# Optimization experiments

Measured on AMD Instinct MI355X. Metric: run time of the kernel, lower is better.

The kernel has to match this reference:

```python
import jax, jax.numpy as jnp
import numpy as np

T, R, L = 3, 4, 2            # node types, edge relations, HGT layers
H, D = 8, 16                 # heads, head dim
OUT = H * D                  # 128
IN = 128
N_T = 30000                  # nodes per type
E = 200000                   # edges per relation
EDGE_SRC = (0, 0, 1, 0)      # src node type of each relation
EDGE_DST = (0, 1, 0, 2)      # dst node type of each relation


def segment_softmax(logits, seg, num_seg):
    # softmax over edges grouped by destination node (per head)
    m = jax.ops.segment_max(logits, seg, num_segments=num_seg)
    m = jnp.where(jnp.isfinite(m), m, 0.0)
    e = jnp.exp(logits - m[seg])
    ssum = jax.ops.segment_sum(e, seg, num_segments=num_seg)
    return e / (ssum[seg] + 1e-16)


def hgt_layer(hs, edge_index, k_w, k_b, q_w, q_b, v_w, v_b, a_w, a_b, skip, a_rel, m_rel, p_rel):
    # per-node-type K/Q/V projections, [N_t, H, D]
    k = [(hs[t] @ k_w[t] + k_b[t]).reshape(-1, H, D) for t in range(T)]
    q = [(hs[t] @ q_w[t] + q_b[t]).reshape(-1, H, D) for t in range(T)]
    v = [(hs[t] @ v_w[t] + v_b[t]).reshape(-1, H, D) for t in range(T)]
    agg = [jnp.zeros((hs[t].shape[0], OUT), hs[t].dtype) for t in range(T)]
    inv_sqrt_d = 1.0 / np.sqrt(D).astype(np.float32)
    for r in range(R):
        s, d = EDGE_SRC[r], EDGE_DST[r]
        src, dst = edge_index[r, 0], edge_index[r, 1]
        # relation-specific transforms of source K and V
        k_rel = jnp.einsum('nhd,hde->nhe', k[s], a_rel[r])
        v_rel = jnp.einsum('nhd,hde->nhe', v[s], m_rel[r])
        k_j = k_rel[src]           # [E, H, D]
        v_j = v_rel[src]           # [E, H, D]
        q_i = q[d][dst]            # [E, H, D]
        logits = (q_i * k_j).sum(-1) * p_rel[r] * inv_sqrt_d   # [E, H]
        n_d = hs[d].shape[0]
        alpha = segment_softmax(logits, dst, n_d)              # [E, H]
        msg = (v_j * alpha[..., None]).reshape(-1, OUT)        # [E, OUT]
        agg[d] = agg[d] + jax.ops.segment_sum(msg, dst, num_segments=n_d)
    out = []
    for t in range(T):
        o = jax.nn.gelu(agg[t], approximate=False) @ a_w[t] + a_b[t]
        a_s = jax.nn.sigmoid(skip[t])
        out.append(a_s * o + (1.0 - a_s) * hs[t])   # learnable skip (dims match)
    return out


def _forward(x_t0, x_t1, x_t2, x_homo, lin_w, lin_b, k_w, k_b, q_w, q_b, v_w, v_b,
             a_w, a_b, skip, a_rel, m_rel, p_rel, edge_index, node_type_argmax):
    xs = [x_t0, x_t1, x_t2]
    # type-specific input projection + ReLU
    hs = [jax.nn.relu(xs[t] @ lin_w[t] + lin_b[t]) for t in range(T)]
    for l in range(L):
        hs = hgt_layer(hs, edge_index, k_w[l], k_b[l], q_w[l], q_b[l], v_w[l], v_b[l],
                       a_w[l], a_b[l], skip[l], a_rel[l], m_rel[l], p_rel[l])
    # hetero_to_homo_features: scatter per-type rows back to global node order
    num_nodes = x_homo.shape[0]
    h = jnp.zeros((num_nodes, OUT), hs[0].dtype)
    for t in range(T):
        mask = node_type_argmax == t
        local = jnp.clip(jnp.cumsum(mask) - 1, 0, hs[t].shape[0] - 1)
        h = jnp.where(mask[:, None], hs[t][local], h)
    return h


def setup_inputs() -> dict:
    key = jax.random.key(0)
    ks = jax.random.split(key, 16)
    w = 0.05
    return {
        'x_t0': jax.random.normal(ks[0], (N_T, IN), jnp.float32),
        'x_t1': jax.random.normal(ks[1], (N_T, IN), jnp.float32),
        'x_t2': jax.random.normal(ks[2], (N_T, IN), jnp.float32),
        'x_homo': jax.random.normal(ks[3], (T * N_T, IN), jnp.float32),
        'lin_w': jax.random.normal(ks[4], (T, IN, OUT), jnp.float32) * w,
        'lin_b': jnp.zeros((T, OUT), jnp.float32),
        'k_w': jax.random.normal(ks[5], (L, T, OUT, OUT), jnp.float32) * w,
        'k_b': jnp.zeros((L, T, OUT), jnp.float32),
        'q_w': jax.random.normal(ks[6], (L, T, OUT, OUT), jnp.float32) * w,
        'q_b': jnp.zeros((L, T, OUT), jnp.float32),
        'v_w': jax.random.normal(ks[7], (L, T, OUT, OUT), jnp.float32) * w,
        'v_b': jnp.zeros((L, T, OUT), jnp.float32),
        'a_w': jax.random.normal(ks[8], (L, T, OUT, OUT), jnp.float32) * w,
        'a_b': jnp.zeros((L, T, OUT), jnp.float32),
        'skip': jnp.ones((L, T), jnp.float32),
        'a_rel': jax.random.normal(ks[9], (L, R, H, D, D), jnp.float32) * 0.2,
        'm_rel': jax.random.normal(ks[10], (L, R, H, D, D), jnp.float32) * 0.2,
        'p_rel': jnp.ones((L, R, H), jnp.float32),
        'edge_index': jax.random.randint(ks[11], (R, 2, E), 0, N_T),
        'node_type_argmax': jnp.repeat(jnp.arange(T), N_T),
    }


def reference(x_t0, x_t1, x_t2, x_homo, lin_w, lin_b, k_w, k_b, q_w, q_b, v_w, v_b,
              a_w, a_b, skip, a_rel, m_rel, p_rel, edge_index, node_type_argmax):
    return _forward(x_t0, x_t1, x_t2, x_homo, lin_w, lin_b, k_w, k_b, q_w, q_b,
                    v_w, v_b, a_w, a_b, skip, a_rel, m_rel, p_rel,
                    edge_index, node_type_argmax)
```

## Files before the change

### kernel.cpp

```cpp
#include <hip/hip_runtime.h>
#include <math.h>

#define NT_NODES 30000
#define NE_EDGES 200000
#define NTY 3
#define NRL 4
#define NLY 2
#define NH 8
#define HD 16
#define FDIM 128
#define SCAN_BLOCKS 118

typedef unsigned short u16;
typedef unsigned int u32;
typedef __attribute__((ext_vector_type(8))) short bf16x8;
typedef __attribute__((ext_vector_type(4))) float f32x4;

__device__ __forceinline__ float bf2f(u16 u) {
  return __uint_as_float(((u32)u) << 16);
}
__device__ __forceinline__ u16 f2bf(float f) {
  u32 u = __float_as_uint(f);
  return (u16)((u + 0x7FFFu + ((u >> 16) & 1u)) >> 16);
}

__device__ __forceinline__ float gelu_f(float x) {
  return 0.5f * x * (1.f + erff(x * 0.7071067811865475f));
}

struct WtBatch { const float* w[23]; };
__global__ __launch_bounds__(256) void wt_prep(WtBatch wb, u16* wt) {
  const float* w = wb.w[blockIdx.x];
  u16* o = wt + (size_t)blockIdx.x * FDIM * FDIM;
  for (int i = threadIdx.x; i < FDIM * FDIM; i += 256) {
    int n = i >> 7, k = i & 127;
    o[i] = f2bf(w[(size_t)k * FDIM + n]);
  }
}


struct QkvOut { const u16* WT; const float* bias; u16* C; int ldc; };
struct QkvTask { const u16* A; int nout; QkvOut o[3]; };
struct QkvBatch { QkvTask t[3]; };

__global__ __launch_bounds__(256) void gemm_qkv(QkvBatch gb, int M) {
  const QkvTask tk = gb.t[blockIdx.z];
  const int tid = threadIdx.x;
  const int wv = tid >> 6;
  const int lane = tid & 63;
  const int row0 = blockIdx.x * 64;

  __shared__ u16 As[64 * 128];
  __shared__ u16 Bt[128 * 128];

  #pragma unroll
  for (int i = 0; i < 4; i++) {
    int g = tid + 256 * i;
    int r = g >> 4, k8 = g & 15;
    int grow = row0 + r;
    uint4 v = make_uint4(0, 0, 0, 0);
    if (grow < M) v = *(const uint4*)(tk.A + (size_t)grow * FDIM + k8 * 8);
    *(uint4*)(As + r * 128 + ((k8 ^ (r & 7)) * 8)) = v;
  }
  __syncthreads();

  const int rsel = lane & 15, ksel = lane >> 4;
  bf16x8 af[4][4];
  #pragma unroll
  for (int ks = 0; ks < 4; ks++) {
    int kg = ks * 4 + ksel;
    #pragma unroll
    for (int i = 0; i < 4; i++) {
      int r = 16 * i + rsel;
      af[ks][i] = *(const bf16x8*)(As + r * 128 + ((kg ^ (r & 7)) * 8));
    }
  }

  for (int ot = 0; ot < tk.nout; ot++) {
    const QkvOut oo = tk.o[ot];
    #pragma unroll
    for (int i = 0; i < 8; i++) {
      int g = tid + 256 * i;
      int n = g >> 4, k8 = g & 15;
      uint4 v = *(const uint4*)(oo.WT + (size_t)n * FDIM + k8 * 8);
      *(uint4*)(Bt + n * 128 + ((k8 ^ (n & 7)) * 8)) = v;
    }
    __syncthreads();

    f32x4 acc[4][2] = {};
    #pragma unroll
    for (int ks = 0; ks < 4; ks++) {
      int kg = ks * 4 + ksel;
      bf16x8 bfr[2];
      #pragma unroll
      for (int j = 0; j < 2; j++) {
        int n = 32 * wv + 16 * j + rsel;
        bfr[j] = *(const bf16x8*)(Bt + n * 128 + ((kg ^ (n & 7)) * 8));
      }
      #pragma unroll
      for (int i = 0; i < 4; i++)
        #pragma unroll
        for (int j = 0; j < 2; j++)
          acc[i][j] = __builtin_amdgcn_mfma_f32_16x16x32_bf16(af[ks][i], bfr[j], acc[i][j], 0, 0, 0);
    }

    const int ldc = oo.ldc;
    float bj[2];
    int colj[2];
    #pragma unroll
    for (int j = 0; j < 2; j++) {
      colj[j] = 32 * wv + 16 * j + rsel;
      bj[j] = oo.bias[colj[j]];
    }
    #pragma unroll
    for (int i = 0; i < 4; i++) {
      #pragma unroll
      for (int rr = 0; rr < 4; rr++) {
        int grow = row0 + 16 * i + (lane >> 4) * 4 + rr;
        if (grow >= M) continue;
        #pragma unroll
        for (int j = 0; j < 2; j++)
          oo.C[(size_t)grow * ldc + colj[j]] = f2bf(acc[i][j][rr] + bj[j]);
      }
    }
    __syncthreads();
  }
}

struct GemmTaskF {
  const float* A; const float* A2; const u16* WT; const float* bias;
  float* C; const u16* oldh; const float* skipp;
};
struct GemmBatchF { GemmTaskF t[3]; };

template<int GELU_A, int EPI_SKIP, int RELU, int BF16_OUT>
__global__ __launch_bounds__(256) void gemm_mfma_f(GemmBatchF gb, int M) {
  const GemmTaskF tk = gb.t[blockIdx.z];
  const int tid = threadIdx.x;
  const int wv = tid >> 6;
  const int lane = tid & 63;
  const int row0 = blockIdx.x * 64;

  __shared__ u16 As[64 * 128];
  __shared__ u16 Bt[128 * 128];

  #pragma unroll
  for (int i = 0; i < 4; i++) {
    int g = tid + 256 * i;
    int r = g >> 4, k8 = g & 15;
    int grow = row0 + r;
    float4 va = make_float4(0.f, 0.f, 0.f, 0.f), vb = va;
    if (grow < M) {
      const float* ap = tk.A + (size_t)grow * FDIM + k8 * 8;
      va = *(const float4*)ap;
      vb = *(const float4*)(ap + 4);
      if (GELU_A && tk.A2) {
        const float* ap2 = tk.A2 + (size_t)grow * FDIM + k8 * 8;
        float4 w = *(const float4*)ap2;
        float4 z = *(const float4*)(ap2 + 4);
        va.x += w.x; va.y += w.y; va.z += w.z; va.w += w.w;
        vb.x += z.x; vb.y += z.y; vb.z += z.z; vb.w += z.w;
      }
      if (GELU_A) {
        va.x = gelu_f(va.x); va.y = gelu_f(va.y); va.z = gelu_f(va.z); va.w = gelu_f(va.w);
        vb.x = gelu_f(vb.x); vb.y = gelu_f(vb.y); vb.z = gelu_f(vb.z); vb.w = gelu_f(vb.w);
      }
    }
    u32 w0 = (u32)f2bf(va.x) | ((u32)f2bf(va.y) << 16);
    u32 w1 = (u32)f2bf(va.z) | ((u32)f2bf(va.w) << 16);
    u32 w2 = (u32)f2bf(vb.x) | ((u32)f2bf(vb.y) << 16);
    u32 w3 = (u32)f2bf(vb.z) | ((u32)f2bf(vb.w) << 16);
    u32* dst = (u32*)(As + r * 128 + ((k8 ^ (r & 7)) * 8));
    dst[0] = w0; dst[1] = w1; dst[2] = w2; dst[3] = w3;
  }
  #pragma unroll
  for (int i = 0; i < 8; i++) {
    int g = tid + 256 * i;
    int n = g >> 4, k8 = g & 15;
    uint4 v = *(const uint4*)(tk.WT + (size_t)n * FDIM + k8 * 8);
    *(uint4*)(Bt + n * 128 + ((k8 ^ (n & 7)) * 8)) = v;
  }
  __syncthreads();

  f32x4 acc[4][2] = {};
  const int rsel = lane & 15, ksel = lane >> 4;
  #pragma unroll
  for (int ks = 0; ks < 4; ks++) {
    int kg = ks * 4 + ksel;
    bf16x8 af[4], bfr[2];
    #pragma unroll
    for (int i = 0; i < 4; i++) {
      int r = 16 * i + rsel;
      af[i] = *(const bf16x8*)(As + r * 128 + ((kg ^ (r & 7)) * 8));
    }
    #pragma unroll
    for (int j = 0; j < 2; j++) {
      int n = 32 * wv + 16 * j + rsel;
      bfr[j] = *(const bf16x8*)(Bt + n * 128 + ((kg ^ (n & 7)) * 8));
    }
    #pragma unroll
    for (int i = 0; i < 4; i++)
      #pragma unroll
      for (int j = 0; j < 2; j++)
        acc[i][j] = __builtin_amdgcn_mfma_f32_16x16x32_bf16(af[i], bfr[j], acc[i][j], 0, 0, 0);
  }

  float a_s = 0.f, b_s = 0.f;
  if (EPI_SKIP) { a_s = 1.f / (1.f + expf(-tk.skipp[0])); b_s = 1.f - a_s; }
  float bj[2];
  int colj[2];
  #pragma unroll
  for (int j = 0; j < 2; j++) {
    colj[j] = 32 * wv + 16 * j + rsel;
    bj[j] = tk.bias[colj[j]];
  }
  #pragma unroll
  for (int i = 0; i < 4; i++) {
    #pragma unroll
    for (int rr = 0; rr < 4; rr++) {
      int grow = row0 + 16 * i + (lane >> 4) * 4 + rr;
      if (grow >= M) continue;
      #pragma unroll
      for (int j = 0; j < 2; j++) {
        float v = acc[i][j][rr] + bj[j];
        if (RELU) v = fmaxf(v, 0.f);
        if (EPI_SKIP) v = a_s * v + b_s * bf2f(tk.oldh[(size_t)grow * FDIM + colj[j]]);
        if (BF16_OUT) ((u16*)tk.C)[(size_t)grow * FDIM + colj[j]] = f2bf(v);
        else tk.C[(size_t)grow * FDIM + colj[j]] = v;
      }
    }
  }
}

__global__ __launch_bounds__(256) void csr_hist(const int* __restrict__ edge_index,
                                                int* __restrict__ counts) {
  int idx = blockIdx.x * 256 + threadIdx.x;
  if (idx >= NRL * NE_EDGES) return;
  int r = idx / NE_EDGES, e = idx - r * NE_EDGES;
  int d = edge_index[(size_t)(r * 2 + 1) * NE_EDGES + e];
  atomicAdd(&counts[r * NT_NODES + d], 1);
}

__global__ __launch_bounds__(256) void scan_block(const int* __restrict__ counts,
                                                  int* __restrict__ off,
                                                  int* __restrict__ aux) {
  int r = blockIdx.y, b = blockIdx.x, t = threadIdx.x;
  int i = b * 256 + t;
  int v = (i < NT_NODES) ? counts[r * NT_NODES + i] : 0;
  __shared__ int lds[256];
  lds[t] = v;
  __syncthreads();
  #pragma unroll
  for (int dlt = 1; dlt < 256; dlt <<= 1) {
    int x = (t >= dlt) ? lds[t - dlt] : 0;
    __syncthreads();
    lds[t] += x;
    __syncthreads();
  }
  if (i < NT_NODES) off[(size_t)r * (NT_NODES + 1) + i] = lds[t] - v;
  if (t == 255) aux[r * SCAN_BLOCKS + b] = lds[255];
}

__global__ __launch_bounds__(128) void scan_aux(const int* __restrict__ aux,
                                                int* __restrict__ auxe,
                                                int* __restrict__ off) {
  int r = blockIdx.x, t = threadIdx.x;
  __shared__ int lds[128];
  int v = (t < SCAN_BLOCKS) ? aux[r * SCAN_BLOCKS + t] : 0;
  lds[t] = v;
  __syncthreads();
  #pragma unroll
  for (int dlt = 1; dlt < 128; dlt <<= 1) {
    int x = (t >= dlt) ? lds[t - dlt] : 0;
    __syncthreads();
    lds[t] += x;
    __syncthreads();
  }
  if (t < SCAN_BLOCKS) auxe[r * SCAN_BLOCKS + t] = lds[t] - v;
  if (t == 127) off[(size_t)r * (NT_NODES + 1) + NT_NODES] = lds[127];
}

__global__ __launch_bounds__(256) void scan_add(const int* __restrict__ auxe,
                                                int* __restrict__ off,
                                                int* __restrict__ cursor) {
  int r = blockIdx.y, b = blockIdx.x, t = threadIdx.x;
  int i = b * 256 + t;
  if (i >= NT_NODES) return;
  int val = off[(size_t)r * (NT_NODES + 1) + i] + auxe[r * SCAN_BLOCKS + b];
  off[(size_t)r * (NT_NODES + 1) + i] = val;
  cursor[r * NT_NODES + i] = val;
}

__global__ __launch_bounds__(256) void csr_scatter(const int* __restrict__ edge_index,
                                                   int* __restrict__ cursor,
                                                   int* __restrict__ csr_src) {
  int idx = blockIdx.x * 256 + threadIdx.x;
  if (idx >= NRL * NE_EDGES) return;
  int r = idx / NE_EDGES, e = idx - r * NE_EDGES;
  int s = edge_index[(size_t)(r * 2 + 0) * NE_EDGES + e];
  int d = edge_index[(size_t)(r * 2 + 1) * NE_EDGES + e];
  int pos = atomicAdd(&cursor[r * NT_NODES + d], 1);
  csr_src[(size_t)r * NE_EDGES + pos] = s;
}

__global__ void csr_pad(int* __restrict__ pad) {
  if (threadIdx.x < 8) pad[threadIdx.x] = 0;
}

struct AttnRel {
  const int* csr_src; const int* off;
  const u16* q;
  const u16* kv;
  const float* Arel;
  const float* Mrel;
  const float* prel;
  float* agg;
};
struct AttnBatch { AttnRel r[4]; };

__global__ __launch_bounds__(256) void attn_fused(AttnBatch ab) {
  const AttnRel rp = ab.r[blockIdx.y];
  const int wave = threadIdx.x >> 6;
  const int lane = threadIdx.x & 63;
  const int d = blockIdx.x * 2 + (wave >> 1);
  if (d >= NT_NODES) return;
  const int hf = wave & 1;
  const int cl = lane & 15;
  const int gh = hf * 4 + (lane >> 4);
  const int grp = lane & ~15;
  const int el = lane & 7;

  float qv = bf2f(rp.q[(size_t)d * FDIM + hf * 64 + lane]);
  const float* A = rp.Arel + (size_t)gh * 256;
  float qp = 0.f;
  #pragma unroll
  for (int ee = 0; ee < 16; ee++) {
    float qe = __shfl(qv, grp + ee, 64);
    qp += A[cl * 16 + ee] * qe;
  }
  qp *= rp.prel[gh] * 0.25f;

  const u16* KV = rp.kv;
  const int* __restrict__ cs = rp.csr_src;
  int lo = rp.off[d], hi = rp.off[d + 1];
  lo = __builtin_amdgcn_readfirstlane(lo);
  hi = __builtin_amdgcn_readfirstlane(hi);
  const size_t koff = hf * 64 + lane;
  const size_t voff = 128 + hf * 64 + lane;
  float acc = 0.f, ssum = 0.f;
  for (int pos = lo; pos < hi; pos += 8) {
    int s0 = cs[pos + 0], s1 = cs[pos + 1], s2 = cs[pos + 2], s3 = cs[pos + 3];
    int s4 = cs[pos + 4], s5 = cs[pos + 5], s6 = cs[pos + 6], s7 = cs[pos + 7];
    u16 k0 = KV[(size_t)s0 * 256 + koff], k1 = KV[(size_t)s1 * 256 + koff];
    u16 k2 = KV[(size_t)s2 * 256 + koff], k3 = KV[(size_t)s3 * 256 + koff];
    u16 k4 = KV[(size_t)s4 * 256 + koff], k5 = KV[(size_t)s5 * 256 + koff];
    u16 k6 = KV[(size_t)s6 * 256 + koff], k7 = KV[(size_t)s7 * 256 + koff];
    u16 v0 = KV[(size_t)s0 * 256 + voff], v1 = KV[(size_t)s1 * 256 + voff];
    u16 v2 = KV[(size_t)s2 * 256 + voff], v3 = KV[(size_t)s3 * 256 + voff];
    u16 v4 = KV[(size_t)s4 * 256 + voff], v5 = KV[(size_t)s5 * 256 + voff];
    u16 v6 = KV[(size_t)s6 * 256 + voff], v7 = KV[(size_t)s7 * 256 + voff];
    float p0 = qp * bf2f(k0), p1 = qp * bf2f(k1);
    float p2 = qp * bf2f(k2), p3 = qp * bf2f(k3);
    float p4 = qp * bf2f(k4), p5 = qp * bf2f(k5);
    float p6 = qp * bf2f(k6), p7 = qp * bf2f(k7);
    float s01 = (lane & 1) ? p0 : p1, c01 = (lane & 1) ? p1 : p0;
    float s23 = (lane & 1) ? p2 : p3, c23 = (lane & 1) ? p3 : p2;
    float s45 = (lane & 1) ? p4 : p5, c45 = (lane & 1) ? p5 : p4;
    float s67 = (lane & 1) ? p6 : p7, c67 = (lane & 1) ? p7 : p6;
    float r01 = c01 + __shfl_xor(s01, 1, 64);
    float r23 = c23 + __shfl_xor(s23, 1, 64);
    float r45 = c45 + __shfl_xor(s45, 1, 64);
    float r67 = c67 + __shfl_xor(s67, 1, 64);
    float sA = (lane & 2) ? r01 : r23, cA = (lane & 2) ? r23 : r01;
    float sB = (lane & 2) ? r45 : r67, cB = (lane & 2) ? r67 : r45;
    float rA = cA + __shfl_xor(sA, 2, 64);
    float rB = cB + __shfl_xor(sB, 2, 64);
    float sC = (lane & 4) ? rA : rB, cC = (lane & 4) ? rB : rA;
    float rF = cC + __shfl_xor(sC, 4, 64);
    rF += __shfl_xor(rF, 8, 64);
    int rem = hi - pos;
    float e = (el < rem) ? __expf(rF) : 0.f;
    float e0 = __shfl(e, grp + 0, 64), e1 = __shfl(e, grp + 1, 64);
    float e2 = __shfl(e, grp + 2, 64), e3 = __shfl(e, grp + 3, 64);
    float e4 = __shfl(e, grp + 4, 64), e5 = __shfl(e, grp + 5, 64);
    float e6 = __shfl(e, grp + 6, 64), e7 = __shfl(e, grp + 7, 64);
    acc += e0 * bf2f(v0) + e1 * bf2f(v1) + e2 * bf2f(v2) + e3 * bf2f(v3)
         + e4 * bf2f(v4) + e5 * bf2f(v5) + e6 * bf2f(v6) + e7 * bf2f(v7);
    ssum += ((e0 + e1) + (e2 + e3)) + ((e4 + e5) + (e6 + e7));
  }
  float inv = 1.f / (ssum + 1e-16f);
  float S = acc * inv;

  const float* M = rp.Mrel + (size_t)gh * 256;
  float o = 0.f;
  #pragma unroll
  for (int d2 = 0; d2 < 16; d2++) {
    float sv = __shfl(S, grp + d2, 64);
    o += sv * M[d2 * 16 + cl];
  }
  rp.agg[(size_t)d * FDIM + hf * 64 + lane] = o;
}

__global__ __launch_bounds__(256) void scatter_out(const float* h0, const float* h1,
                                                   const float* h2, const int* ntype,
                                                   float* out, int NN) {
  int idx = blockIdx.x * 256 + threadIdx.x;
  if (idx >= NN * 32) return;
  int i = idx >> 5, c4 = idx & 31;
  int t = ntype[i];
  const float* hp = (t == 0) ? h0 : ((t == 1) ? h1 : h2);
  int local = i - t * NT_NODES;
  ((float4*)out)[idx] = ((const float4*)hp)[(size_t)local * 32 + c4];
}

static const int ESRC[NRL] = {0, 0, 1, 0};
static const int EDST[NRL] = {0, 1, 0, 2};

extern "C" void kernel_launch(void* const* d_in, const int* in_sizes, int n_in,
                              void* d_out, int out_size, void* d_ws, size_t ws_size,
                              hipStream_t stream) {
  const float* x[3] = {(const float*)d_in[0], (const float*)d_in[1], (const float*)d_in[2]};
  const float* lin_w = (const float*)d_in[4];
  const float* lin_b = (const float*)d_in[5];
  const float* k_w   = (const float*)d_in[6];
  const float* k_b   = (const float*)d_in[7];
  const float* q_w   = (const float*)d_in[8];
  const float* q_b   = (const float*)d_in[9];
  const float* v_w   = (const float*)d_in[10];
  const float* v_b   = (const float*)d_in[11];
  const float* a_w   = (const float*)d_in[12];
  const float* a_b   = (const float*)d_in[13];
  const float* skip  = (const float*)d_in[14];
  const float* a_rel = (const float*)d_in[15];
  const float* m_rel = (const float*)d_in[16];
  const float* p_rel = (const float*)d_in[17];
  const int* edge_index = (const int*)d_in[18];
  const int* ntype   = (const int*)d_in[19];
  float* out = (float*)d_out;

  const size_t NF = (size_t)NT_NODES * FDIM;
  float* p = (float*)d_ws;
  auto alloc = [&](size_t n) { float* r = p; p += n; return r; };
  float* bufA = alloc(3 * NF);
  float* bufB = alloc(3 * NF);
  float* agg  = alloc(3 * NF);
  float* aggX = alloc(NF);
  u16* kv0 = (u16*)alloc(NF);
  u16* kv1 = (u16*)alloc(NF);
  u16* wt  = (u16*)alloc(23 * FDIM * FDIM / 2);
  int* counts  = (int*)(p);
  int* cursor  = counts + NRL * NT_NODES;
  int* offsets = cursor + NRL * NT_NODES;
  int* aux     = offsets + NRL * (NT_NODES + 1);
  int* auxe    = aux + NRL * SCAN_BLOCKS;
  int* csr_src = auxe + NRL * SCAN_BLOCKS;

  const int gemm_gx = (NT_NODES + 63) / 64;

  {
    WtBatch wb{};
    for (int l = 0; l < NLY; l++) {
      for (int t = 0; t < 3; t++)
        wb.w[l * 7 + t] = q_w + (size_t)(l * NTY + t) * FDIM * FDIM;
      wb.w[l * 7 + 3] = k_w + (size_t)(l * NTY + 0) * FDIM * FDIM;
      wb.w[l * 7 + 4] = v_w + (size_t)(l * NTY + 0) * FDIM * FDIM;
      wb.w[l * 7 + 5] = k_w + (size_t)(l * NTY + 1) * FDIM * FDIM;
      wb.w[l * 7 + 6] = v_w + (size_t)(l * NTY + 1) * FDIM * FDIM;
    }
    for (int t = 0; t < 3; t++)
      wb.w[14 + t] = lin_w + (size_t)t * FDIM * FDIM;
    for (int l = 0; l < NLY; l++)
      for (int t = 0; t < 3; t++)
        wb.w[17 + l * 3 + t] = a_w + (size_t)(l * NTY + t) * FDIM * FDIM;
    wt_prep<<<dim3(23), 256, 0, stream>>>(wb, wt);
  }

  hipMemsetAsync(counts, 0, NRL * NT_NODES * sizeof(int), stream);
  csr_hist<<<dim3((NRL * NE_EDGES + 255) / 256), 256, 0, stream>>>(edge_index, counts);
  scan_block<<<dim3(SCAN_BLOCKS, NRL), 256, 0, stream>>>(counts, offsets, aux);
  scan_aux<<<dim3(NRL), 128, 0, stream>>>(aux, auxe, offsets);
  scan_add<<<dim3(SCAN_BLOCKS, NRL), 256, 0, stream>>>(auxe, offsets, cursor);
  csr_scatter<<<dim3((NRL * NE_EDGES + 255) / 256), 256, 0, stream>>>(edge_index, cursor, csr_src);
  csr_pad<<<dim3(1), 64, 0, stream>>>(csr_src + (size_t)NRL * NE_EDGES);

  {
    GemmBatchF gb{};
    for (int t = 0; t < 3; t++) {
      gb.t[t].A = x[t];
      gb.t[t].A2 = nullptr;
      gb.t[t].WT = wt + (size_t)(14 + t) * FDIM * FDIM;
      gb.t[t].bias = lin_b + (size_t)t * FDIM;
      gb.t[t].C = (float*)((u16*)bufA + (size_t)t * NF);
      gb.t[t].oldh = nullptr; gb.t[t].skipp = nullptr;
    }
    gemm_mfma_f<0, 0, 1, 1><<<dim3(gemm_gx, 1, 3), 256, 0, stream>>>(gb, NT_NODES);
  }

  float* cur = bufA;
  float* alt = bufB;
  for (int l = 0; l < NLY; l++) {
    u16* qbf = (u16*)alt;
    const u16* hb = (const u16*)cur;

    {
      QkvBatch gb{};
      gb.t[0].A = hb;  gb.t[0].nout = 3;
      gb.t[0].o[0] = { wt + (size_t)(l * 7 + 0) * FDIM * FDIM, q_b + (size_t)(l * NTY + 0) * FDIM, qbf,            FDIM };
      gb.t[0].o[1] = { wt + (size_t)(l * 7 + 3) * FDIM * FDIM, k_b + (size_t)(l * NTY + 0) * FDIM, kv0,            256 };
      gb.t[0].o[2] = { wt + (size_t)(l * 7 + 4) * FDIM * FDIM, v_b + (size_t)(l * NTY + 0) * FDIM, kv0 + 128,      256 };
      gb.t[1].A = hb + NF;  gb.t[1].nout = 3;
      gb.t[1].o[0] = { wt + (size_t)(l * 7 + 1) * FDIM * FDIM, q_b + (size_t)(l * NTY + 1) * FDIM, qbf + NF,       FDIM };
      gb.t[1].o[1] = { wt + (size_t)(l * 7 + 5) * FDIM * FDIM, k_b + (size_t)(l * NTY + 1) * FDIM, kv1,            256 };
      gb.t[1].o[2] = { wt + (size_t)(l * 7 + 6) * FDIM * FDIM, v_b + (size_t)(l * NTY + 1) * FDIM, kv1 + 128,      256 };
      gb.t[2].A = hb + 2 * NF;  gb.t[2].nout = 1;
      gb.t[2].o[0] = { wt + (size_t)(l * 7 + 2) * FDIM * FDIM, q_b + (size_t)(l * NTY + 2) * FDIM, qbf + 2 * NF,   FDIM };
      gemm_qkv<<<dim3(gemm_gx, 1, 3), 256, 0, stream>>>(gb, NT_NODES);
    }

    {
      AttnBatch ab{};
      for (int r = 0; r < NRL; r++) {
        int dt = EDST[r];
        ab.r[r].csr_src = csr_src + (size_t)r * NE_EDGES;
        ab.r[r].off  = offsets + (size_t)r * (NT_NODES + 1);
        ab.r[r].q    = qbf + (size_t)dt * NF;
        ab.r[r].kv   = (ESRC[r] == 0) ? kv0 : kv1;
        ab.r[r].Arel = a_rel + (size_t)(l * NRL + r) * NH * HD * HD;
        ab.r[r].Mrel = m_rel + (size_t)(l * NRL + r) * NH * HD * HD;
        ab.r[r].prel = p_rel + (size_t)(l * NRL + r) * NH;
        ab.r[r].agg  = (r == 2) ? aggX : (agg + (size_t)dt * NF);
      }
      attn_fused<<<dim3((NT_NODES + 1) / 2, NRL), 256, 0, stream>>>(ab);
    }

    {
      GemmBatchF gb{};
      for (int t = 0; t < 3; t++) {
        gb.t[t].A = agg + (size_t)t * NF;
        gb.t[t].A2 = (t == 0) ? aggX : nullptr;
        gb.t[t].WT = wt + (size_t)(17 + l * 3 + t) * FDIM * FDIM;
        gb.t[t].bias = a_b + (size_t)(l * NTY + t) * FDIM;
        gb.t[t].oldh = hb + (size_t)t * NF;
        gb.t[t].skipp = skip + (size_t)(l * NTY + t);
        if (l == 0) gb.t[t].C = (float*)((u16*)alt + (size_t)t * NF);
        else        gb.t[t].C = alt + (size_t)t * NF;
      }
      if (l == 0) gemm_mfma_f<1, 1, 0, 1><<<dim3(gemm_gx, 1, 3), 256, 0, stream>>>(gb, NT_NODES);
      else        gemm_mfma_f<1, 1, 0, 0><<<dim3(gemm_gx, 1, 3), 256, 0, stream>>>(gb, NT_NODES);
    }
    float* tmp = cur; cur = alt; alt = tmp;
  }

  const int NN = 3 * NT_NODES;
  scatter_out<<<dim3((NN * 32 + 255) / 256), 256, 0, stream>>>(
      cur, cur + NF, cur + 2 * NF, ntype, out, NN);
}
```

Measured before the change: 575.8 us.

## Fold relation attention matrix and prior scale into per-relation Q weights

A new prep kernel multiplies each destination-type Q weight and bias by the relation-specific a_rel matrix and scales it by p_rel/sqrt(D). This produces one fused Q projection per relation. The QKV GEMM now emits four Q outputs, with type 0 producing two of them, and the attention kernel reads the pre-transformed query directly. That drops its per-node shuffle-based 16x16 matvec and its reads of a_rel and p_rel. In exchange it adds one extra 128-wide GEMM output per layer and a larger Q buffer, and the folded weights are rounded to bf16 after the product, which slightly changes numerics.

```diff
diff --git a/kernel.cpp b/kernel.cpp
--- a/kernel.cpp
+++ b/kernel.cpp
@@ -38,9 +38,50 @@
   }
 }
 
+__global__ __launch_bounds__(256) void qfuse(const float* __restrict__ q_w,
+                                             const float* __restrict__ q_b,
+                                             const float* __restrict__ a_rel,
+                                             const float* __restrict__ p_rel,
+                                             u16* __restrict__ wqp,
+                                             float* __restrict__ bqp) {
+  const int lr = blockIdx.x;
+  const int l = lr >> 2, r = lr & 3;
+  const int dt = (r == 1) ? 1 : ((r == 3) ? 2 : 0);
+  const float* qw = q_w + (size_t)(l * NTY + dt) * FDIM * FDIM;
+  const float* qb = q_b + (size_t)(l * NTY + dt) * FDIM;
+  const float* A  = a_rel + (size_t)(l * NRL + r) * NH * HD * HD;
+  const float* pr = p_rel + (size_t)(l * NRL + r) * NH;
+  u16* wo = wqp + (size_t)lr * FDIM * FDIM;
+  float* bo = bqp + (size_t)lr * FDIM;
+
+  __shared__ float As[NH * HD * HD];
+  __shared__ float sh[NH];
+  for (int i = threadIdx.x; i < NH * HD * HD; i += 256) As[i] = A[i];
+  if (threadIdx.x < NH) sh[threadIdx.x] = pr[threadIdx.x] * 0.25f;
+  __syncthreads();
+
+  for (int i = threadIdx.x; i < FDIM * FDIM; i += 256) {
+    int n = i >> 7, k = i & 127;
+    int h = n >> 4, cl = n & 15;
+    float s = 0.f;
+    #pragma unroll
+    for (int ee = 0; ee < HD; ee++)
+      s += qw[(size_t)k * FDIM + h * HD + ee] * As[h * HD * HD + cl * HD + ee];
+    wo[(size_t)n * FDIM + k] = f2bf(s * sh[h]);
+  }
+  if (threadIdx.x < FDIM) {
+    int n = threadIdx.x, h = n >> 4, cl = n & 15;
+    float s = 0.f;
+    #pragma unroll
+    for (int ee = 0; ee < HD; ee++)
+      s += qb[h * HD + ee] * As[h * HD * HD + cl * HD + ee];
+    bo[n] = s * sh[h];
+  }
+}
+
 
 struct QkvOut { const u16* WT; const float* bias; u16* C; int ldc; };
-struct QkvTask { const u16* A; int nout; QkvOut o[3]; };
+struct QkvTask { const u16* A; int nout; QkvOut o[4]; };
 struct QkvBatch { QkvTask t[3]; };
 
 __global__ __launch_bounds__(256) void gemm_qkv(QkvBatch gb, int M) {
@@ -311,9 +352,7 @@
   const int* csr_src; const int* off;
   const u16* q;
   const u16* kv;
-  const float* Arel;
   const float* Mrel;
-  const float* prel;
   float* agg;
 };
 struct AttnBatch { AttnRel r[4]; };
@@ -330,15 +369,7 @@
   const int grp = lane & ~15;
   const int el = lane & 7;
 
-  float qv = bf2f(rp.q[(size_t)d * FDIM + hf * 64 + lane]);
-  const float* A = rp.Arel + (size_t)gh * 256;
-  float qp = 0.f;
-  #pragma unroll
-  for (int ee = 0; ee < 16; ee++) {
-    float qe = __shfl(qv, grp + ee, 64);
-    qp += A[cl * 16 + ee] * qe;
-  }
-  qp *= rp.prel[gh] * 0.25f;
+  float qp = bf2f(rp.q[(size_t)d * FDIM + hf * 64 + lane]);
 
   const u16* KV = rp.kv;
   const int* __restrict__ cs = rp.csr_src;
@@ -448,6 +479,8 @@
   u16* kv0 = (u16*)alloc(NF);
   u16* kv1 = (u16*)alloc(NF);
   u16* wt  = (u16*)alloc(23 * FDIM * FDIM / 2);
+  u16* wqp = (u16*)alloc(8 * FDIM * FDIM / 2);
+  float* bqp = alloc(8 * FDIM);
   int* counts  = (int*)(p);
   int* cursor  = counts + NRL * NT_NODES;
   int* offsets = cursor + NRL * NT_NODES;
@@ -473,6 +506,7 @@
       for (int t = 0; t < 3; t++)
         wb.w[17 + l * 3 + t] = a_w + (size_t)(l * NTY + t) * FDIM * FDIM;
     wt_prep<<<dim3(23), 256, 0, stream>>>(wb, wt);
+    qfuse<<<dim3(NLY * NRL), 256, 0, stream>>>(q_w, q_b, a_rel, p_rel, wqp, bqp);
   }
 
   hipMemsetAsync(counts, 0, NRL * NT_NODES * sizeof(int), stream);
@@ -504,31 +538,30 @@
 
     {
       QkvBatch gb{};
-      gb.t[0].A = hb;  gb.t[0].nout = 3;
-      gb.t[0].o[0] = { wt + (size_t)(l * 7 + 0) * FDIM * FDIM, q_b + (size_t)(l * NTY + 0) * FDIM, qbf,            FDIM };
-      gb.t[0].o[1] = { wt + (size_t)(l * 7 + 3) * FDIM * FDIM, k_b + (size_t)(l * NTY + 0) * FDIM, kv0,            256 };
-      gb.t[0].o[2] = { wt + (size_t)(l * 7 + 4) * FDIM * FDIM, v_b + (size_t)(l * NTY + 0) * FDIM, kv0 + 128,      256 };
+      gb.t[0].A = hb;  gb.t[0].nout = 4;
+      gb.t[0].o[0] = { wqp + (size_t)(l * 4 + 0) * FDIM * FDIM, bqp + (size_t)(l * 4 + 0) * FDIM, qbf + 0 * NF, FDIM };
+      gb.t[0].o[1] = { wqp + (size_t)(l * 4 + 2) * FDIM * FDIM, bqp + (size_t)(l * 4 + 2) * FDIM, qbf + 2 * NF, FDIM };
+      gb.t[0].o[2] = { wt + (size_t)(l * 7 + 3) * FDIM * FDIM, k_b + (size_t)(l * NTY + 0) * FDIM, kv0,       256 };
+      gb.t[0].o[3] = { wt + (size_t)(l * 7 + 4) * FDIM * FDIM, v_b + (size_t)(l * NTY + 0) * FDIM, kv0 + 128, 256 };
       gb.t[1].A = hb + NF;  gb.t[1].nout = 3;
-      gb.t[1].o[0] = { wt + (size_t)(l * 7 + 1) * FDIM * FDIM, q_b + (size_t)(l * NTY + 1) * FDIM, qbf + NF,       FDIM };
-      gb.t[1].o[1] = { wt + (size_t)(l * 7 + 5) * FDIM * FDIM, k_b + (size_t)(l * NTY + 1) * FDIM, kv1,            256 };
-      gb.t[1].o[2] = { wt + (size_t)(l * 7 + 6) * FDIM * FDIM, v_b + (size_t)(l * NTY + 1) * FDIM, kv1 + 128,      256 };
+      gb.t[1].o[0] = { wqp + (size_t)(l * 4 + 1) * FDIM * FDIM, bqp + (size_t)(l * 4 + 1) * FDIM, qbf + 1 * NF, FDIM };
+      gb.t[1].o[1] = { wt + (size_t)(l * 7 + 5) * FDIM * FDIM, k_b + (size_t)(l * NTY + 1) * FDIM, kv1,       256 };
+      gb.t[1].o[2] = { wt + (size_t)(l * 7 + 6) * FDIM * FDIM, v_b + (size_t)(l * NTY + 1) * FDIM, kv1 + 128, 256 };
       gb.t[2].A = hb + 2 * NF;  gb.t[2].nout = 1;
-      gb.t[2].o[0] = { wt + (size_t)(l * 7 + 2) * FDIM * FDIM, q_b + (size_t)(l * NTY + 2) * FDIM, qbf + 2 * NF,   FDIM };
+      gb.t[2].o[0] = { wqp + (size_t)(l * 4 + 3) * FDIM * FDIM, bqp + (size_t)(l * 4 + 3) * FDIM, qbf + 3 * NF, FDIM };
       gemm_qkv<<<dim3(gemm_gx, 1, 3), 256, 0, stream>>>(gb, NT_NODES);
     }
 
     {
       AttnBatch ab{};
       for (int r = 0; r < NRL; r++) {
-        int dt = EDST[r];
+        int dt = EDST[r]; (void)dt;
         ab.r[r].csr_src = csr_src + (size_t)r * NE_EDGES;
         ab.r[r].off  = offsets + (size_t)r * (NT_NODES + 1);
-        ab.r[r].q    = qbf + (size_t)dt * NF;
+        ab.r[r].q    = qbf + (size_t)r * NF;
         ab.r[r].kv   = (ESRC[r] == 0) ? kv0 : kv1;
-        ab.r[r].Arel = a_rel + (size_t)(l * NRL + r) * NH * HD * HD;
         ab.r[r].Mrel = m_rel + (size_t)(l * NRL + r) * NH * HD * HD;
-        ab.r[r].prel = p_rel + (size_t)(l * NRL + r) * NH;
-        ab.r[r].agg  = (r == 2) ? aggX : (agg + (size_t)dt * NF);
+        ab.r[r].agg  = (r == 2) ? aggX : (agg + (size_t)EDST[r] * NF);
       }
       attn_fused<<<dim3((NT_NODES + 1) / 2, NRL), 256, 0, stream>>>(ab);
     }
```

After: 553.0 us. 4.0% less time.
